# Performance work log

Measured on AMD Instinct MI355X. Metric: run time of the kernel, lower is better.

## Reference

```python
import jax, jax.numpy as jnp
import numpy as np


def setup_inputs() -> dict:
    key = jax.random.key(0)
    ks = jax.random.split(key, 8)
    B, Cin, Cattr, Cout, H, W = 8, 256, 256, 256, 64, 64
    x = jax.random.normal(ks[0], (B, Cin, H, W), dtype=jnp.float32)
    attr = jax.random.normal(ks[1], (B, Cattr, H, W), dtype=jnp.float32)
    # 1x1 conv weights stored as [out, in] (kernel_size=1 squeezed)
    sq = 1.0 / np.sqrt(Cin)
    sa = 1.0 / np.sqrt(Cattr)
    Wq = jax.random.uniform(ks[2], (Cout, Cin), jnp.float32, -sq, sq)
    bq = jax.random.uniform(ks[3], (Cout,), jnp.float32, -sq, sq)
    Wk = jax.random.uniform(ks[4], (Cout, Cattr), jnp.float32, -sa, sa)
    bk = jax.random.uniform(ks[5], (Cout,), jnp.float32, -sa, sa)
    Wv = jax.random.uniform(ks[6], (Cout, Cattr), jnp.float32, -sa, sa)
    bv = jax.random.uniform(ks[7], (Cout,), jnp.float32, -sa, sa)
    return {"x": x, "attr": attr, "Wq": Wq, "bq": bq, "Wk": Wk, "bk": bk, "Wv": Wv, "bv": bv}


def reference(x, attr, Wq, bq, Wk, bk, Wv, bv):
    B, Cin, H, W = x.shape
    # 1x1 convs == per-pixel linear projections
    q = jnp.einsum('bchw,oc->bohw', x, Wq) + bq[None, :, None, None]      # [B,C,H,W]
    k = jnp.einsum('bchw,oc->bohw', attr, Wk) + bk[None, :, None, None]
    v = jnp.einsum('bchw,oc->bohw', attr, Wv) + bv[None, :, None, None]
    C = q.shape[1]
    qf = q.reshape(B, C, H * W)   # [B,C,N]
    kf = k.reshape(B, C, H * W)
    vf = v.reshape(B, C, H * W)
    # attn[b,i,j] = sum_c q[b,c,i] * k[b,c,j]  -> softmax over j
    attn = jax.nn.softmax(jnp.einsum('bci,bcj->bij', qf, kf), axis=-1)    # [B,N,N]
    out = jnp.einsum('bcj,bij->bci', vf, attn)                            # [B,C,N]
    return out.reshape(B, C, H, W) + x
```

## Files before the change

kernel.cpp:

```cpp
#include <hip/hip_runtime.h>

typedef _Float16 f16;
typedef _Float16 f16x8 __attribute__((ext_vector_type(8)));
typedef _Float16 f16x4 __attribute__((ext_vector_type(4)));
typedef float f32x4 __attribute__((ext_vector_type(4)));
typedef float f32x16 __attribute__((ext_vector_type(16)));

#define LOG2E 1.44269504088896340736f
#define SOFF  36.0f
#define CDIM 256
#define NPIX 4096

__device__ __forceinline__ void gl2lds16(const f16* g, const f16* l) {
    __builtin_amdgcn_global_load_lds((const __attribute__((address_space(1))) unsigned int*)g,
                                     (__attribute__((address_space(3))) unsigned int*)l, 16, 0, 0);
}

__global__ void convert_w_kernel(const float* __restrict__ Wq, const float* __restrict__ Wk,
                                 const float* __restrict__ Wv,
                                 f16* __restrict__ WqF, f16* __restrict__ WkF,
                                 f16* __restrict__ WvF) {
    int t = blockIdx.x * 256 + threadIdx.x;
    int m = t >> 13;
    int g = t & 8191;
    int lane = g & 63;
    int ksct = g >> 6;
    int ks = ksct & 15, ct = ksct >> 4;
    int o = ct * 32 + (lane & 31);
    int cin0 = ks * 16 + (lane >> 5) * 8;
    const float* W = (m == 0) ? Wq : ((m == 1) ? Wk : Wv);
    f16* WF = (m == 0) ? WqF : ((m == 1) ? WkF : WvF);
    const float scale = (m == 0) ? LOG2E : 1.0f;
    const float* src = W + (size_t)o * CDIM + cin0;
    f16x8 v;
#pragma unroll
    for (int e = 0; e < 8; ++e) v[e] = (f16)(src[e] * scale);
    *(f16x8*)(WF + (size_t)g * 8) = v;
}

__global__ __launch_bounds__(256, 2)
void proj_kernel(const float* __restrict__ x, const float* __restrict__ attr,
                 const f16* __restrict__ WqF, const float* __restrict__ bq,
                 const f16* __restrict__ WkF, const float* __restrict__ bk,
                 const f16* __restrict__ WvF, const float* __restrict__ bv,
                 f16* __restrict__ qT, f16* __restrict__ kC, f16* __restrict__ vW) {
    __shared__ __align__(16) f16 Xs[64 * 256];
    __shared__ __align__(16) f16 As[64 * 256];
    __shared__ __align__(16) f16 Ostage[4][1024];

    const int b  = blockIdx.x & 7;
    const int i0 = (blockIdx.x >> 3) * 64;
    const int t  = threadIdx.x;
    const int w = t >> 6, lane = t & 63, l31 = lane & 31, hi = lane >> 5;
    const int xu  = (l31 >> 1) & 15;
    const int hib = (hi ^ (l31 & 1)) * 8;

    {
        const int i  = t & 63;
        const int cb = t >> 6;
        const float* xb = x    + (size_t)b * CDIM * NPIX + i0 + i;
        const float* ab = attr + (size_t)b * CDIM * NPIX + i0 + i;
#pragma unroll 2
        for (int rep = 0; rep < 8; ++rep) {
            int chunk = cb * 8 + rep;
            const float* xs = xb + (size_t)(chunk * 8) * NPIX;
            const float* as_ = ab + (size_t)(chunk * 8) * NPIX;
            f16x8 xv, av;
#pragma unroll
            for (int e = 0; e < 8; ++e) {
                xv[e] = (f16)xs[(size_t)e * NPIX];
                av[e] = (f16)as_[(size_t)e * NPIX];
            }
            int phys = chunk ^ (i & 31);
            *(f16x8*)(Xs + i * 256 + phys * 8) = xv;
            *(f16x8*)(As + i * 256 + phys * 8) = av;
        }
    }
    __syncthreads();

#pragma unroll 1
    for (int k = 0; k < 12; ++k) {
        const int tt = w + 4 * k;
        const int kind = tt >> 4;
        const int rr = tt & 15;
        const int ct = rr >> 1;
        const int half = rr & 1;

        const f16* WF = (kind == 0) ? WqF : ((kind == 1) ? WkF : WvF);
        const f16* Bs = (kind == 0) ? Xs : As;
        const float* bias = (kind == 0) ? bq : ((kind == 1) ? bk : bv);
        const float bscale = (kind == 0) ? LOG2E : 1.0f;

        const f16* ap = WF + (size_t)(ct * 16) * 512 + (size_t)lane * 8;
        const f16* bp = Bs + (half * 32 + l31) * 256 + hib;

        f32x16 acc;
#pragma unroll
        for (int r = 0; r < 16; ++r) acc[r] = 0.0f;
#pragma unroll
        for (int ks = 0; ks < 16; ++ks) {
            f16x8 afr = *(const f16x8*)(ap + ks * 512);
            f16x8 bfr = *(const f16x8*)(bp + ((ks ^ xu) << 4));
            acc = __builtin_amdgcn_mfma_f32_32x32x16_f16(afr, bfr, acc, 0, 0, 0);
        }

        f16* st = Ostage[w];
        if (kind < 2) {
#pragma unroll
            for (int g = 0; g < 4; ++g) {
                f32x4 bb = *(const f32x4*)(bias + ct * 32 + 4 * hi + 8 * g);
                f16x4 pk;
#pragma unroll
                for (int e = 0; e < 4; ++e) pk[e] = (f16)(acc[4 * g + e] + bb[e] * bscale);
                *(f16x4*)(st + l31 * 32 + 4 * hi + 8 * g) = pk;
            }
            if (kind == 0) {
                f16* dst = qT + ((size_t)b * NPIX + i0 + half * 32) * CDIM + ct * 32;
#pragma unroll
                for (int d = 0; d < 2; ++d) {
                    int row = d * 16 + (lane >> 2);
                    int c8  = (lane & 3) * 8;
                    f16x8 v = *(const f16x8*)(st + row * 32 + c8);
                    *(f16x8*)(dst + (size_t)row * CDIM + c8) = v;
                }
            } else {
                const int j0 = i0 + half * 32;
                f16* dstb = kC + (size_t)b * CDIM * NPIX;
#pragma unroll
                for (int d = 0; d < 2; ++d) {
                    int row = d * 16 + (lane >> 2);
                    int kl  = lane & 3;
                    f16x8 v = *(const f16x8*)(st + row * 32 + kl * 8);
                    *(f16x8*)(dstb + ((size_t)(ct * 4 + kl) * NPIX + j0 + row) * 8) = v;
                }
            }
        } else {
#pragma unroll
            for (int g = 0; g < 4; ++g) {
                f32x4 bb = *(const f32x4*)(bias + ct * 32 + 4 * hi + 8 * g);
#pragma unroll
                for (int e = 0; e < 4; ++e) {
                    int c31 = 4 * hi + 8 * g + e;
                    st[c31 * 32 + l31] = (f16)(acc[4 * g + e] + bb[e]);
                }
            }
            const int j0 = i0 + half * 32;
            f16* dstb = vW + (size_t)b * CDIM * NPIX + (size_t)(ct * 32) * NPIX + j0;
#pragma unroll
            for (int d = 0; d < 2; ++d) {
                int chunk = d * 64 + lane;
                int c31 = chunk >> 2, jch = chunk & 3;
                *(f16x8*)(dstb + (size_t)c31 * NPIX + jch * 8) =
                    *(const f16x8*)(st + chunk * 8);
            }
        }
    }
}

__global__ __launch_bounds__(512, 2)
void attn_kernel(const f16* __restrict__ qT, const f16* __restrict__ kC,
                 const f16* __restrict__ vW, const float* __restrict__ x,
                 float* __restrict__ out) {
    extern __shared__ unsigned char smem[];

    const int b    = blockIdx.x & 7;
    const int i0   = (blockIdx.x >> 3) * 128;
    const int t    = threadIdx.x;
    const int w    = t >> 6;
    const int lane = t & 63;
    const int l31  = lane & 31;
    const int hi   = lane >> 5;
    const int iw   = (w & 3) * 32;
    const int jh   = (w >> 2) * 32;
    const int jh8  = (w >> 2) * 4;
    const int ig   = i0 + iw + l31;

    f16x8 qf[16];
    {
        const f16* qp = qT + ((size_t)b * NPIX + ig) * CDIM + hi * 8;
#pragma unroll
        for (int ks = 0; ks < 16; ++ks) qf[ks] = *(const f16x8*)(qp + ks * 16);
    }

    const int kbase = hi * 512 + (jh >> 5) * 256 + l31 * 8;
    int vp2o[2];
    {
        int vbase = 16384 + (l31 & 7) * 256 + ((l31 >> 3) << 6);
#pragma unroll
        for (int kj = 0; kj < 2; ++kj)
            vp2o[kj] = vbase + (((jh8 + 2 * kj + hi) ^ (l31 & 7)) << 3);
    }

    f32x16 acc[8];
#pragma unroll
    for (int ct = 0; ct < 8; ++ct)
#pragma unroll
        for (int r = 0; r < 16; ++r) acc[ct][r] = 0.0f;
    float lrun = 0.0f;

    const f16* kb = kC + (size_t)b * CDIM * NPIX;
    const f16* vb = vW + (size_t)b * CDIM * NPIX;
    f16* lds0 = (f16*)smem;
    const int wub = (t & ~63) * 8;

    {
#pragma unroll
        for (int rep = 0; rep < 4; ++rep) {
            int slot = t + rep * 512;
            int kc = slot >> 6, jhalf = (slot >> 5) & 1, pj = slot & 31;
            gl2lds16(kb + ((size_t)kc * NPIX + jhalf * 32 + pj) * 8,
                     lds0 + wub + rep * 4096);
            int row = slot >> 5, pv = slot & 31;
            int vc = ((row >> 3) << 5) | (((pv >> 3) & 3) << 3) | (row & 7);
            int vjc = (pv & 7) ^ (row & 7);
            gl2lds16(vb + (size_t)vc * NPIX + vjc * 8,
                     lds0 + 16384 + wub + rep * 4096);
        }
    }

    union Q4 { f16x4 h; unsigned int u[2]; };
    union B8 { f16x8 h; unsigned int u[4]; };

#pragma unroll 1
    for (int jt = 0; jt < 64; ++jt) {
        const int p = jt & 1;
        __syncthreads();

        if (jt < 63) {
            const int j0n = (jt + 1) * 64;
            f16* dstb = lds0 + (p ^ 1) * 32768;
#pragma unroll
            for (int rep = 0; rep < 4; ++rep) {
                int slot = t + rep * 512;
                int kc = slot >> 6, jhalf = (slot >> 5) & 1, pj = slot & 31;
                gl2lds16(kb + ((size_t)kc * NPIX + j0n + jhalf * 32 + pj) * 8,
                         dstb + wub + rep * 4096);
                int row = slot >> 5, pv = slot & 31;
                int vc = ((row >> 3) << 5) | (((pv >> 3) & 3) << 3) | (row & 7);
                int vjc = (pv & 7) ^ (row & 7);
                gl2lds16(vb + (size_t)vc * NPIX + j0n + vjc * 8,
                         dstb + 16384 + wub + rep * 4096);
            }
        }

        const f16* L = lds0 + p * 32768;

        f32x16 s;
#pragma unroll
        for (int r = 0; r < 16; ++r) s[r] = -SOFF;
#pragma unroll
        for (int ks = 0; ks < 16; ++ks)
            s = __builtin_amdgcn_mfma_f32_32x32x16_f16(
                *(const f16x8*)(L + kbase + ks * 1024), qf[ks], s, 0, 0, 0);

        Q4 ownq[4];
        float rtot = 0.0f;
#pragma unroll
        for (int g = 0; g < 4; ++g) {
            float p0 = __builtin_amdgcn_exp2f(s[4 * g + 0]);
            float p1 = __builtin_amdgcn_exp2f(s[4 * g + 1]);
            float p2 = __builtin_amdgcn_exp2f(s[4 * g + 2]);
            float p3 = __builtin_amdgcn_exp2f(s[4 * g + 3]);
            rtot += (p0 + p1) + (p2 + p3);
            ownq[g].h[0] = (f16)p0; ownq[g].h[1] = (f16)p1;
            ownq[g].h[2] = (f16)p2; ownq[g].h[3] = (f16)p3;
        }
        lrun += rtot;

        f16x8 pb[2];
#pragma unroll
        for (int kj = 0; kj < 2; ++kj) {
            int sidx = 2 * kj + 1 - hi;
            int oidx = 2 * kj + hi;
            unsigned int s0 = ownq[sidx].u[0], s1 = ownq[sidx].u[1];
            unsigned int r0 = (unsigned int)__shfl_xor((int)s0, 32);
            unsigned int r1 = (unsigned int)__shfl_xor((int)s1, 32);
            B8 bb;
            bb.u[0] = hi ? r0 : ownq[oidx].u[0];
            bb.u[1] = hi ? r1 : ownq[oidx].u[1];
            bb.u[2] = hi ? ownq[oidx].u[0] : r0;
            bb.u[3] = hi ? ownq[oidx].u[1] : r1;
            pb[kj] = bb.h;
        }

#pragma unroll
        for (int ct = 0; ct < 8; ++ct) {
            acc[ct] = __builtin_amdgcn_mfma_f32_32x32x16_f16(
                *(const f16x8*)(L + vp2o[0] + ct * 2048), pb[0], acc[ct], 0, 0, 0);
            acc[ct] = __builtin_amdgcn_mfma_f32_32x32x16_f16(
                *(const f16x8*)(L + vp2o[1] + ct * 2048), pb[1], acc[ct], 0, 0, 0);
        }
    }

    float lsum = lrun + __shfl_xor(lrun, 32);
    __syncthreads();
    float* Obuf = (float*)smem;
    float* Ls   = (float*)(smem + 131072);
    if (w >= 4) {
        float* ob = Obuf + (w - 4) * 8192;
#pragma unroll
        for (int ct = 0; ct < 8; ++ct)
#pragma unroll
            for (int r = 0; r < 16; ++r) {
                int c = ct * 32 + (r & 3) + 8 * (r >> 2) + 4 * hi;
                ob[c * 32 + l31] = acc[ct][r];
            }
        if (hi == 0) Ls[(w - 4) * 32 + l31] = lsum;
    }
    __syncthreads();
    if (w < 4) {
        const float ltot = lsum + Ls[w * 32 + l31];
        const float invl = 1.0f / ltot;
        const float* po = Obuf + w * 8192;
        const float* xb = x + (size_t)b * CDIM * NPIX + i0 + iw;
        float* og = out + (size_t)b * CDIM * NPIX + i0 + iw;
#pragma unroll
        for (int ct = 0; ct < 8; ++ct)
#pragma unroll
            for (int r = 0; r < 16; ++r) {
                int c = ct * 32 + (r & 3) + 8 * (r >> 2) + 4 * hi;
                size_t off = (size_t)c * NPIX + l31;
                og[off] = (acc[ct][r] + po[c * 32 + l31]) * invl + xb[off];
            }
    }
}

extern "C" void kernel_launch(void* const* d_in, const int* in_sizes, int n_in,
                              void* d_out, int out_size, void* d_ws, size_t ws_size,
                              hipStream_t stream) {
    const float* x    = (const float*)d_in[0];
    const float* attr = (const float*)d_in[1];
    const float* Wq   = (const float*)d_in[2];
    const float* bq   = (const float*)d_in[3];
    const float* Wk   = (const float*)d_in[4];
    const float* bk   = (const float*)d_in[5];
    const float* Wv   = (const float*)d_in[6];
    const float* bv   = (const float*)d_in[7];
    float* out = (float*)d_out;

    char* ws = (char*)d_ws;
    const size_t qkv_bytes = (size_t)8 * NPIX * CDIM * sizeof(f16);
    f16* qT   = (f16*)ws;
    f16* kC   = (f16*)(ws + qkv_bytes);
    f16* vW   = (f16*)(ws + 2 * qkv_bytes);
    f16* WqF  = (f16*)(ws + 3 * qkv_bytes);
    f16* WkF  = WqF + 65536;
    f16* WvF  = WkF + 65536;

    (void)hipFuncSetAttribute((const void*)attn_kernel,
                              hipFuncAttributeMaxDynamicSharedMemorySize, 131584);

    convert_w_kernel<<<96, 256, 0, stream>>>(Wq, Wk, Wv, WqF, WkF, WvF);
    proj_kernel<<<512, 256, 0, stream>>>(x, attr, WqF, bq, WkF, bk, WvF, bv, qT, kC, vW);
    attn_kernel<<<256, 512, 131584, stream>>>(qT, kC, vW, x, out);
}
```

Before: 296.1 us.

## Software-pipeline the attention loop: overlap QK^T of tile j with PV of tile j-1

```diff
diff --git a/kernel.cpp b/kernel.cpp
--- a/kernel.cpp
+++ b/kernel.cpp
@@ -185,7 +185,7 @@
     const int kbase = hi * 512 + (jh >> 5) * 256 + l31 * 8;
     int vp2o[2];
     {
-        int vbase = 16384 + (l31 & 7) * 256 + ((l31 >> 3) << 6);
+        int vbase = (l31 & 7) * 256 + ((l31 >> 3) << 6);
 #pragma unroll
         for (int kj = 0; kj < 2; ++kj)
             vp2o[kj] = vbase + (((jh8 + 2 * kj + hi) ^ (l31 & 7)) << 3);
@@ -210,48 +210,60 @@
             int kc = slot >> 6, jhalf = (slot >> 5) & 1, pj = slot & 31;
             gl2lds16(kb + ((size_t)kc * NPIX + jhalf * 32 + pj) * 8,
                      lds0 + wub + rep * 4096);
-            int row = slot >> 5, pv = slot & 31;
-            int vc = ((row >> 3) << 5) | (((pv >> 3) & 3) << 3) | (row & 7);
-            int vjc = (pv & 7) ^ (row & 7);
-            gl2lds16(vb + (size_t)vc * NPIX + vjc * 8,
-                     lds0 + 16384 + wub + rep * 4096);
         }
     }
 
     union Q4 { f16x4 h; unsigned int u[2]; };
     union B8 { f16x8 h; unsigned int u[4]; };
+    f16x8 pbp[2];
 
 #pragma unroll 1
     for (int jt = 0; jt < 64; ++jt) {
         const int p = jt & 1;
         __syncthreads();
 
-        if (jt < 63) {
+        {
+            f16* kdst = lds0 + (p ^ 1) * 16384 + wub;
+            f16* vdst = lds0 + 32768 + p * 16384 + wub;
             const int j0n = (jt + 1) * 64;
-            f16* dstb = lds0 + (p ^ 1) * 32768;
+            const int j0v = jt * 64;
 #pragma unroll
             for (int rep = 0; rep < 4; ++rep) {
                 int slot = t + rep * 512;
-                int kc = slot >> 6, jhalf = (slot >> 5) & 1, pj = slot & 31;
-                gl2lds16(kb + ((size_t)kc * NPIX + j0n + jhalf * 32 + pj) * 8,
-                         dstb + wub + rep * 4096);
+                if (jt < 63) {
+                    int kc = slot >> 6, jhalf = (slot >> 5) & 1, pj = slot & 31;
+                    gl2lds16(kb + ((size_t)kc * NPIX + j0n + jhalf * 32 + pj) * 8,
+                             kdst + rep * 4096);
+                }
                 int row = slot >> 5, pv = slot & 31;
                 int vc = ((row >> 3) << 5) | (((pv >> 3) & 3) << 3) | (row & 7);
                 int vjc = (pv & 7) ^ (row & 7);
-                gl2lds16(vb + (size_t)vc * NPIX + j0n + vjc * 8,
-                         dstb + 16384 + wub + rep * 4096);
-            }
-        }
-
-        const f16* L = lds0 + p * 32768;
+                gl2lds16(vb + (size_t)vc * NPIX + j0v + vjc * 8,
+                         vdst + rep * 4096);
+            }
+        }
+
+        const f16* Lk = lds0 + p * 16384;
+        const f16* Lv = lds0 + 32768 + (p ^ 1) * 16384;
 
         f32x16 s;
 #pragma unroll
         for (int r = 0; r < 16; ++r) s[r] = -SOFF;
-#pragma unroll
-        for (int ks = 0; ks < 16; ++ks)
-            s = __builtin_amdgcn_mfma_f32_32x32x16_f16(
-                *(const f16x8*)(L + kbase + ks * 1024), qf[ks], s, 0, 0, 0);
+        if (jt > 0) {
+#pragma unroll
+            for (int ks = 0; ks < 16; ++ks) {
+                s = __builtin_amdgcn_mfma_f32_32x32x16_f16(
+                    *(const f16x8*)(Lk + kbase + ks * 1024), qf[ks], s, 0, 0, 0);
+                int kj = ks >> 3, ct = ks & 7;
+                acc[ct] = __builtin_amdgcn_mfma_f32_32x32x16_f16(
+                    *(const f16x8*)(Lv + vp2o[kj] + ct * 2048), pbp[kj], acc[ct], 0, 0, 0);
+            }
+        } else {
+#pragma unroll
+            for (int ks = 0; ks < 16; ++ks)
+                s = __builtin_amdgcn_mfma_f32_32x32x16_f16(
+                    *(const f16x8*)(Lk + kbase + ks * 1024), qf[ks], s, 0, 0, 0);
+        }
 
         Q4 ownq[4];
         float rtot = 0.0f;
@@ -267,7 +279,6 @@
         }
         lrun += rtot;
 
-        f16x8 pb[2];
 #pragma unroll
         for (int kj = 0; kj < 2; ++kj) {
             int sidx = 2 * kj + 1 - hi;
@@ -280,15 +291,19 @@
             bb.u[1] = hi ? r1 : ownq[oidx].u[1];
             bb.u[2] = hi ? ownq[oidx].u[0] : r0;
             bb.u[3] = hi ? ownq[oidx].u[1] : r1;
-            pb[kj] = bb.h;
-        }
-
+            pbp[kj] = bb.h;
+        }
+    }
+
+    __syncthreads();
+    {
+        const f16* Lv = lds0 + 32768 + 16384;
 #pragma unroll
         for (int ct = 0; ct < 8; ++ct) {
             acc[ct] = __builtin_amdgcn_mfma_f32_32x32x16_f16(
-                *(const f16x8*)(L + vp2o[0] + ct * 2048), pb[0], acc[ct], 0, 0, 0);
+                *(const f16x8*)(Lv + vp2o[0] + ct * 2048), pbp[0], acc[ct], 0, 0, 0);
             acc[ct] = __builtin_amdgcn_mfma_f32_32x32x16_f16(
-                *(const f16x8*)(L + vp2o[1] + ct * 2048), pb[1], acc[ct], 0, 0, 0);
+                *(const f16x8*)(Lv + vp2o[1] + ct * 2048), pbp[1], acc[ct], 0, 0, 0);
         }
     }
 
```

Result: slower. 1.037 ms (+250.2%).
